# Kernel optimization log

Hardware: AMD Instinct MI355X
Metric: run time of the kernel (lower is better)

Reference implementation:

```python
import jax, jax.numpy as jnp
import numpy as np

L1 = 1536
L2 = 15
L3 = 64
COUNT = 8
B = 16384


def setup_inputs() -> dict:
    key = jax.random.key(0)
    ks = jax.random.split(key, 10)
    d_in = 2 * L1 // 2  # 1536
    s1 = 1.0 / np.sqrt(d_in)
    s2 = 1.0 / np.sqrt(2 * L2)
    s3 = 1.0 / np.sqrt(L3)
    return {
        "x": jax.random.normal(ks[0], (B, d_in), dtype=jnp.float32),
        "ls_indices": jax.random.randint(ks[1], (B,), 0, COUNT, dtype=jnp.int32),
        "W1": jax.random.uniform(ks[2], (COUNT * (L2 + 1), d_in), jnp.float32, -s1, s1),
        "b1": jax.random.uniform(ks[3], (COUNT * (L2 + 1),), jnp.float32, -s1, s1),
        "Wf": jax.random.uniform(ks[4], (L2 + 1, d_in), jnp.float32, -s1, s1),
        "bf": jax.random.uniform(ks[5], (L2 + 1,), jnp.float32, -s1, s1),
        "W2": jax.random.uniform(ks[6], (COUNT * L3, 2 * L2), jnp.float32, -s2, s2),
        "b2": jax.random.uniform(ks[7], (COUNT * L3,), jnp.float32, -s2, s2),
        "Wo": jax.random.uniform(ks[8], (COUNT, L3), jnp.float32, -s3, s3),
        "bo": jax.random.uniform(ks[9], (COUNT,), jnp.float32, -s3, s3),
    }


def reference(x, ls_indices, W1, b1, Wf, bf, W2, b2, Wo, bo):
    count = Wo.shape[0]
    n = x.shape[0]
    idx = ls_indices[:, None, None]  # [B,1,1] selects the per-sample stack

    # l1: all stacks, then gather selected stack row per sample
    l1s = (x @ W1.T + b1).reshape(n, count, L2 + 1)          # [B, count, 16]
    l1f = x @ Wf.T + bf                                       # [B, 16]
    l1c = jnp.take_along_axis(l1s, idx, axis=1)[:, 0]         # [B, 16]

    l1c_, l1c_out = l1c[:, :L2], l1c[:, L2:]                  # [B,15], [B,1]
    l1f_, l1f_out = l1f[:, :L2], l1f[:, L2:]
    l1x = l1c_ + l1f_
    # squared-clipped-ReLU concat: [pow(x,2)*127/128, x] clamped to [0,1]
    l1x = jnp.clip(jnp.concatenate([l1x * l1x * (127.0 / 128.0), l1x], axis=1), 0.0, 1.0)  # [B,30]

    l2s = (l1x @ W2.T + b2).reshape(n, count, L3)             # [B, count, 64]
    l2c = jnp.take_along_axis(l2s, idx, axis=1)[:, 0]         # [B, 64]
    l2x = jnp.clip(l2c, 0.0, 1.0)

    l3s = (l2x @ Wo.T + bo).reshape(n, count, 1)              # [B, count, 1]
    l3c = jnp.take_along_axis(l3s, idx, axis=1)[:, 0]         # [B, 1]
    return l3c + l1f_out + l1c_out
```

## Files before the change

kernel.cpp:

```cpp
#include <hip/hip_runtime.h>
#include <hip/hip_bf16.h>
#include <stdint.h>

#define L1DIM  1536
#define NOUT   144
#define NSPLIT 2
#define KSPL   768
#define CHUNK  256
#define NCHNK  3
#define STEPS  24
#define LROW   260
#define ROWS   16384
#define PCOLS  32

typedef __bf16 bf16;
typedef __bf16 bf16x8 __attribute__((ext_vector_type(8)));
typedef float  floatx4 __attribute__((ext_vector_type(4)));

__global__ void pack_weights(const float* __restrict__ W1,
                             const float* __restrict__ Wf,
                             bf16* __restrict__ pw) {
    int t = blockIdx.x * blockDim.x + threadIdx.x;
    if (t >= NOUT * 192) return;
    int n = t / 192;
    int o = t % 192;
    const float* src = (n < 128) ? (W1 + (size_t)n * L1DIM + o * 8)
                                 : (Wf + (size_t)(n - 128) * L1DIM + o * 8);
    float4 s0 = ((const float4*)src)[0];
    float4 s1 = ((const float4*)src)[1];
    bf16x8 v;
    v[0] = (bf16)s0.x; v[1] = (bf16)s0.y; v[2] = (bf16)s0.z; v[3] = (bf16)s0.w;
    v[4] = (bf16)s1.x; v[5] = (bf16)s1.y; v[6] = (bf16)s1.z; v[7] = (bf16)s1.w;
    *(bf16x8*)(pw + ((size_t)o * NOUT + n) * 8) = v;
}

__device__ __forceinline__ bf16x8 cvt8(float4 a, float4 b) {
    bf16x8 r;
    r[0] = (bf16)a.x; r[1] = (bf16)a.y; r[2] = (bf16)a.z; r[3] = (bf16)a.w;
    r[4] = (bf16)b.x; r[5] = (bf16)b.y; r[6] = (bf16)b.z; r[7] = (bf16)b.w;
    return r;
}

__global__ __launch_bounds__(512, 2) void gemm_l1(
    const float* __restrict__ x, const int* __restrict__ lsidx,
    const bf16* __restrict__ pw, float* __restrict__ pt)
{
    __shared__ float law[8][16][LROW];

    const int tid  = threadIdx.x;
    const int wv   = tid >> 6;
    const int ln   = tid & 63;
    const int quad = ln >> 4;
    const int lm   = ln & 15;

    const int q   = blockIdx.x >> 7;
    const int blk = blockIdx.x & 127;
    const int rA  = blk * 128 + wv * 16;

    const float* xbase = x + (size_t)rA * L1DIM + q * KSPL;
    float* lw = &law[wv][0][0];

    {
        float4 av[16];
#pragma unroll
        for (int r = 0; r < 16; r++)
            av[r] = *(const float4*)(xbase + (size_t)r * L1DIM + ln * 4);
#pragma unroll
        for (int r = 0; r < 16; r++)
            *(float4*)(lw + r * LROW + ln * 4) = av[r];
    }

    floatx4 acc[9];
#pragma unroll
    for (int i = 0; i < 9; i++) acc[i] = (floatx4){0.f, 0.f, 0.f, 0.f};

    const bf16* pb0 = pw + (((size_t)q * 96 + quad) * NOUT + lm) * 8;
    bf16x8 bcur[9];
#pragma unroll
    for (int t = 0; t < 9; t++)
        bcur[t] = *(const bf16x8*)(pb0 + t * 16 * 8);

    for (int c = 0; c < NCHNK; c++) {
        float4 av2[16];
        if (c < NCHNK - 1) {
#pragma unroll
            for (int r = 0; r < 16; r++)
                av2[r] = *(const float4*)(xbase + (size_t)r * L1DIM
                                          + (c + 1) * CHUNK + ln * 4);
        }
#pragma unroll
        for (int s = 0; s < 8; s++) {
            const int st = c * 8 + s;
            bf16x8 bnxt[9];
            if (st < STEPS - 1) {
                const bf16* pn = pw + (((size_t)q * 96 + (st + 1) * 4 + quad) * NOUT + lm) * 8;
#pragma unroll
                for (int t = 0; t < 9; t++)
                    bnxt[t] = *(const bf16x8*)(pn + t * 16 * 8);
            }
            const float* ap = lw + lm * LROW + s * 32 + quad * 8;
            float4 a0 = *(const float4*)ap;
            float4 a1 = *(const float4*)(ap + 4);
            bf16x8 af = cvt8(a0, a1);
#pragma unroll
            for (int t = 0; t < 9; t++)
                acc[t] = __builtin_amdgcn_mfma_f32_16x16x32_bf16(af, bcur[t], acc[t], 0, 0, 0);
            if (st < STEPS - 1) {
#pragma unroll
                for (int t = 0; t < 9; t++) bcur[t] = bnxt[t];
            }
        }
        if (c < NCHNK - 1) {
#pragma unroll
            for (int r = 0; r < 16; r++)
                *(float4*)(lw + r * LROW + ln * 4) = av2[r];
        }
    }

#pragma unroll
    for (int rp = 0; rp < 4; rp++) {
        const int row = rA + quad * 4 + rp;
        const int bkt = lsidx[row];
        float csel = acc[0][rp];
#pragma unroll
        for (int t = 1; t < 8; t++) csel = (bkt == t) ? acc[t][rp] : csel;
        float* dst = pt + ((size_t)q * ROWS + row) * PCOLS;
        dst[lm]      = csel;
        dst[16 + lm] = acc[8][rp];
    }
}

__global__ __launch_bounds__(256) void epilogue(
    const float* __restrict__ pt, const int* __restrict__ lsidx,
    const float* __restrict__ b1, const float* __restrict__ bf_,
    const float* __restrict__ W2, const float* __restrict__ b2,
    const float* __restrict__ Wo, const float* __restrict__ bo,
    float* __restrict__ out)
{
    __shared__ float ep[32][33];

    const int tid = threadIdx.x;
    const int er  = tid >> 3;
    const int sub = tid & 7;
    const int row = blockIdx.x * 32 + er;

    float4 s = {0.f, 0.f, 0.f, 0.f};
#pragma unroll
    for (int q = 0; q < NSPLIT; q++) {
        float4 v = *(const float4*)&pt[((size_t)q * ROWS + row) * PCOLS + sub * 4];
        s.x += v.x; s.y += v.y; s.z += v.z; s.w += v.w;
    }
    *(float4*)&ep[er][sub * 4] = s;
    __syncthreads();

    const int bkt = lsidx[row];
    const float l1c15 = ep[er][15] + b1[bkt * 16 + 15];
    const float l1f15 = ep[er][31] + bf_[15];

    float l1x[30];
#pragma unroll
    for (int j = 0; j < 15; j++) {
        float tj = (ep[er][j] + b1[bkt * 16 + j]) + (ep[er][16 + j] + bf_[j]);
        float sq = tj * tj * (127.0f / 128.0f);
        l1x[j]      = fminf(fmaxf(sq, 0.f), 1.f);
        l1x[15 + j] = fminf(fmaxf(tj, 0.f), 1.f);
    }

    float part = 0.f;
#pragma unroll
    for (int o = 0; o < 8; o++) {
        const int oi = bkt * 64 + sub * 8 + o;
        const float2* wrow = (const float2*)(W2 + oi * 30);
        float a = b2[oi];
#pragma unroll
        for (int j2 = 0; j2 < 15; j2++) {
            float2 w = wrow[j2];
            a += l1x[2 * j2] * w.x + l1x[2 * j2 + 1] * w.y;
        }
        a = fminf(fmaxf(a, 0.f), 1.f);
        part += a * Wo[oi];
    }
    part += __shfl_xor(part, 1);
    part += __shfl_xor(part, 2);
    part += __shfl_xor(part, 4);
    if (sub == 0) out[row] = part + bo[bkt] + l1c15 + l1f15;
}

extern "C" void kernel_launch(void* const* d_in, const int* in_sizes, int n_in,
                              void* d_out, int out_size, void* d_ws, size_t ws_size,
                              hipStream_t stream) {
    const float* x   = (const float*)d_in[0];
    const int*   idx = (const int*)  d_in[1];
    const float* W1  = (const float*)d_in[2];
    const float* b1  = (const float*)d_in[3];
    const float* Wf  = (const float*)d_in[4];
    const float* bf  = (const float*)d_in[5];
    const float* W2  = (const float*)d_in[6];
    const float* b2  = (const float*)d_in[7];
    const float* Wo  = (const float*)d_in[8];
    const float* bo  = (const float*)d_in[9];
    float* out = (float*)d_out;

    float* pt = (float*)d_ws;
    bf16*  pw = (bf16*)((char*)d_ws + (size_t)NSPLIT * ROWS * PCOLS * 4);

    pack_weights<<<dim3((NOUT * 192 + 255) / 256), dim3(256), 0, stream>>>(W1, Wf, pw);
    gemm_l1<<<dim3(NSPLIT * 128), dim3(512), 0, stream>>>(x, idx, pw, pt);
    epilogue<<<dim3(ROWS / 32), dim3(256), 0, stream>>>(pt, idx, b1, bf, W2, b2, Wo, bo, out);
}
```

Before: 208.3 us.

## Stage activation tiles directly into double-buffered LDS via global_load_lds

The layer-1 GEMM now copies x straight from global memory into shared memory with the async global-to-LDS load builtin, instead of loading into registers and then storing to LDS. Shared memory becomes two buffers per wave, and each chunk shrinks to 128 columns, so the next chunk loads while the current one feeds the MFMAs. This is meant to cut register pressure and the cost of the register-to-LDS store. In exchange, only half the lanes issue the copies, and the explicit vmcnt(0) wait at the end of each chunk also stalls on the prefetched weight loads, which limits overlap.

```diff
diff --git a/kernel.cpp b/kernel.cpp
--- a/kernel.cpp
+++ b/kernel.cpp
@@ -6,10 +6,11 @@
 #define NOUT   144
 #define NSPLIT 2
 #define KSPL   768
-#define CHUNK  256
-#define NCHNK  3
+#define CHUNK  128
+#define CSTEPS 4
+#define NCHNK  6
 #define STEPS  24
-#define LROW   260
+#define LROWF  132
 #define ROWS   16384
 #define PCOLS  32
 
@@ -34,6 +35,12 @@
     *(bf16x8*)(pw + ((size_t)o * NOUT + n) * 8) = v;
 }
 
+__device__ __forceinline__ void gload_lds16(const void* g, void* l) {
+    __builtin_amdgcn_global_load_lds(
+        (const __attribute__((address_space(1))) void*)g,
+        (__attribute__((address_space(3))) void*)l, 16, 0, 0);
+}
+
 __device__ __forceinline__ bf16x8 cvt8(float4 a, float4 b) {
     bf16x8 r;
     r[0] = (bf16)a.x; r[1] = (bf16)a.y; r[2] = (bf16)a.z; r[3] = (bf16)a.w;
@@ -45,7 +52,7 @@
     const float* __restrict__ x, const int* __restrict__ lsidx,
     const bf16* __restrict__ pw, float* __restrict__ pt)
 {
-    __shared__ float law[8][16][LROW];
+    __shared__ float law[8][2][16][LROWF];
 
     const int tid  = threadIdx.x;
     const int wv   = tid >> 6;
@@ -58,47 +65,42 @@
     const int rA  = blk * 128 + wv * 16;
 
     const float* xbase = x + (size_t)rA * L1DIM + q * KSPL;
-    float* lw = &law[wv][0][0];
-
-    {
-        float4 av[16];
-#pragma unroll
-        for (int r = 0; r < 16; r++)
-            av[r] = *(const float4*)(xbase + (size_t)r * L1DIM + ln * 4);
-#pragma unroll
-        for (int r = 0; r < 16; r++)
-            *(float4*)(lw + r * LROW + ln * 4) = av[r];
-    }
+
+    auto stageA = [&](int buf, int c) {
+        if (ln < 32) {
+            const float* g = xbase + c * CHUNK + ln * 4;
+            float* l = &law[wv][buf][0][0] + ln * 4;
+#pragma unroll
+            for (int r = 0; r < 16; r++)
+                gload_lds16(g + (size_t)r * L1DIM, l + r * LROWF);
+        }
+    };
+
+    auto loadB = [&](int st, bf16x8* dst) {
+        const bf16* p = pw + (((size_t)q * 96 + st * 4 + quad) * NOUT + lm) * 8;
+#pragma unroll
+        for (int t = 0; t < 9; t++)
+            dst[t] = *(const bf16x8*)(p + (size_t)t * 16 * 8);
+    };
 
     floatx4 acc[9];
 #pragma unroll
     for (int i = 0; i < 9; i++) acc[i] = (floatx4){0.f, 0.f, 0.f, 0.f};
 
-    const bf16* pb0 = pw + (((size_t)q * 96 + quad) * NOUT + lm) * 8;
+    stageA(0, 0);
+    asm volatile("s_waitcnt vmcnt(0)" ::: "memory");
+
     bf16x8 bcur[9];
-#pragma unroll
-    for (int t = 0; t < 9; t++)
-        bcur[t] = *(const bf16x8*)(pb0 + t * 16 * 8);
+    loadB(0, bcur);
 
     for (int c = 0; c < NCHNK; c++) {
-        float4 av2[16];
-        if (c < NCHNK - 1) {
-#pragma unroll
-            for (int r = 0; r < 16; r++)
-                av2[r] = *(const float4*)(xbase + (size_t)r * L1DIM
-                                          + (c + 1) * CHUNK + ln * 4);
-        }
-#pragma unroll
-        for (int s = 0; s < 8; s++) {
-            const int st = c * 8 + s;
+        if (c < NCHNK - 1) stageA((c + 1) & 1, c + 1);
+#pragma unroll
+        for (int s = 0; s < CSTEPS; s++) {
+            const int st = c * CSTEPS + s;
             bf16x8 bnxt[9];
-            if (st < STEPS - 1) {
-                const bf16* pn = pw + (((size_t)q * 96 + (st + 1) * 4 + quad) * NOUT + lm) * 8;
-#pragma unroll
-                for (int t = 0; t < 9; t++)
-                    bnxt[t] = *(const bf16x8*)(pn + t * 16 * 8);
-            }
-            const float* ap = lw + lm * LROW + s * 32 + quad * 8;
+            if (st < STEPS - 1) loadB(st + 1, bnxt);
+            const float* ap = &law[wv][c & 1][lm][s * 32 + quad * 8];
             float4 a0 = *(const float4*)ap;
             float4 a1 = *(const float4*)(ap + 4);
             bf16x8 af = cvt8(a0, a1);
@@ -110,11 +112,7 @@
                 for (int t = 0; t < 9; t++) bcur[t] = bnxt[t];
             }
         }
-        if (c < NCHNK - 1) {
-#pragma unroll
-            for (int r = 0; r < 16; r++)
-                *(float4*)(lw + r * LROW + ln * 4) = av2[r];
-        }
+        asm volatile("s_waitcnt vmcnt(0)" ::: "memory");
     }
 
 #pragma unroll
```

Measured after the change: 185.6 us. 10.9% less time.
